# Kernel optimization log

Hardware: AMD Instinct MI355X
Metric: run time of the kernel (lower is better)

Reference implementation:

```python
import jax, jax.numpy as jnp
import numpy as np

DIM = 1024
HEADS = 8
DIM_HEAD = 64
EPS = 1e-10
LN_EPS = 1e-5


def setup_inputs() -> dict:
    key = jax.random.key(0)
    k1, k2, k3 = jax.random.split(key, 3)
    b, n = 2, 4096
    x = jax.random.normal(k1, (b, n, DIM), dtype=jnp.float32)
    ln_gamma = jnp.ones((DIM,), dtype=jnp.float32)
    ln_beta = jnp.zeros((DIM,), dtype=jnp.float32)
    w_qkv = jax.random.normal(k2, (DIM, 3 * HEADS * DIM_HEAD), dtype=jnp.float32) * (DIM ** -0.5)
    w_out = jax.random.normal(k3, (HEADS * DIM_HEAD, DIM), dtype=jnp.float32) * ((HEADS * DIM_HEAD) ** -0.5)
    return {"x": x, "ln_gamma": ln_gamma, "ln_beta": ln_beta, "w_qkv": w_qkv, "w_out": w_out}


def _layernorm(x, gamma, beta):
    mu = jnp.mean(x, axis=-1, keepdims=True)
    var = jnp.var(x, axis=-1, keepdims=True)
    return (x - mu) * jax.lax.rsqrt(var + LN_EPS) * gamma + beta


def reference(x, ln_gamma, ln_beta, w_qkv, w_out):
    b, n, _ = x.shape
    h, dh = HEADS, DIM_HEAD
    scale = dh ** -0.5

    xn = _layernorm(x, ln_gamma, ln_beta)          # prenorm
    qkv = xn @ w_qkv                               # [b, n, 3*h*dh]
    q, k, v = jnp.split(qkv, 3, axis=-1)
    # [b, n, h*dh] -> [b, h, n, dh]
    def to_heads(t):
        return t.reshape(b, n, h, dh).transpose(0, 2, 1, 3)
    q, k, v = to_heads(q), to_heads(k), to_heads(v)

    # Ring/blockwise attention with online softmax is mathematically
    # equivalent to full softmax attention with an eps in the denominator.
    sim = jnp.einsum('bhid,bhjd->bhij', q, k) * scale   # [b, h, n, n]
    causal_mask = jnp.tril(jnp.ones((n, n), dtype=bool))
    sim = jnp.where(causal_mask, sim, -jnp.finfo(sim.dtype).max)

    m = jnp.max(sim, axis=-1, keepdims=True)            # row max (stable)
    p = jnp.exp(sim - m)
    denom = jnp.sum(p, axis=-1, keepdims=True) + EPS
    attn = p / denom

    out = jnp.einsum('bhij,bhjd->bhid', attn, v)        # [b, h, n, dh]
    out = out.transpose(0, 2, 1, 3).reshape(b, n, h * dh)
    return out @ w_out                                  # [b, n, dim]
```

## Files before the change

### kernel.cpp

```cpp
#include <hip/hip_runtime.h>
#include <hip/hip_bf16.h>
#include <stdint.h>

typedef unsigned short u16;
typedef unsigned int u32;

typedef __attribute__((ext_vector_type(8))) __bf16 bf16x8;
typedef __attribute__((ext_vector_type(4))) float f32x4;
typedef __attribute__((ext_vector_type(8))) u16 u16x8;

#define DIM 1024
#define SEQ 4096
#define NTOK 8192
#define NBH 16
#define NSLOT 96

static __device__ __forceinline__ float bf2f(u16 u) {
    union { u32 u; float f; } c; c.u = ((u32)u) << 16; return c.f;
}
static __device__ __forceinline__ u16 f2bf(float f) {
    union { float f; u32 u; } c; c.f = f;
    u32 u = c.u;
    return (u16)((u + 0x7FFF + ((u >> 16) & 1)) >> 16);
}
static __device__ __forceinline__ u16 cvt_bf16(float f) {
    union { __bf16 b; u16 u; } c; c.b = (__bf16)f;
    return c.u;
}
static __device__ __forceinline__ f32x4 mfma_bf16(bf16x8 a, bf16x8 b, f32x4 c) {
    return __builtin_amdgcn_mfma_f32_16x16x32_bf16(a, b, c, 0, 0, 0);
}

typedef const __attribute__((address_space(1))) unsigned int* gptr_t;
typedef __attribute__((address_space(3))) unsigned int* lptr_t;

__global__ __launch_bounds__(256) void ln_kernel(const float* __restrict__ x,
                                                 const float* __restrict__ g,
                                                 const float* __restrict__ bta,
                                                 u16* __restrict__ xn) {
    int row = blockIdx.x;
    int tid = threadIdx.x;
    float4 v = ((const float4*)(x + (size_t)row * DIM))[tid];
    float f[4] = {v.x, v.y, v.z, v.w};
    float s = 0.f, s2 = 0.f;
#pragma unroll
    for (int i = 0; i < 4; i++) { s += f[i]; s2 += f[i] * f[i]; }
#pragma unroll
    for (int m = 1; m < 64; m <<= 1) { s += __shfl_xor(s, m); s2 += __shfl_xor(s2, m); }
    __shared__ float red[8];
    int w = tid >> 6;
    if ((tid & 63) == 0) { red[w * 2] = s; red[w * 2 + 1] = s2; }
    __syncthreads();
    s  = red[0] + red[2] + red[4] + red[6];
    s2 = red[1] + red[3] + red[5] + red[7];
    float mu = s * (1.f / DIM);
    float var = s2 * (1.f / DIM) - mu * mu;
    float rstd = rsqrtf(var + 1e-5f);
    u16 o[4];
#pragma unroll
    for (int i = 0; i < 4; i++) {
        int c = tid * 4 + i;
        o[i] = f2bf((f[i] - mu) * rstd * g[c] + bta[c]);
    }
    *(uint64_t*)(xn + (size_t)row * DIM + tid * 4) = *(uint64_t*)o;
}

__global__ __launch_bounds__(256) void transpose_kernel(const float* __restrict__ src,
                                                        u16* __restrict__ dst,
                                                        int R, int C) {
    __shared__ float t[32][33];
    int lx = threadIdx.x & 31, ly = threadIdx.x >> 5;
    int c = blockIdx.x * 32 + lx;
#pragma unroll
    for (int i = 0; i < 32; i += 8)
        t[ly + i][lx] = src[(size_t)(blockIdx.y * 32 + ly + i) * C + c];
    __syncthreads();
    int rr = blockIdx.y * 32 + lx;
#pragma unroll
    for (int i = 0; i < 32; i += 8)
        dst[(size_t)(blockIdx.x * 32 + ly + i) * R + rr] = f2bf(t[lx][ly + i]);
}

template <int K>
static __device__ __forceinline__ void gemm_core(const u16* __restrict__ A,
                                                 const u16* __restrict__ B,
                                                 int rowBase, int colBase,
                                                 u16* A_lds, u16* B_lds,
                                                 f32x4 acc[4][4]) {
    int tid = threadIdx.x;
    int lane = tid & 63;
    int l15 = lane & 15, q4 = lane >> 4;
    int w = tid >> 6;
    int wm = w >> 1, wn = w & 1;
#pragma unroll
    for (int mt = 0; mt < 4; mt++)
#pragma unroll
        for (int nt = 0; nt < 4; nt++) acc[mt][nt] = (f32x4){0.f, 0.f, 0.f, 0.f};

    char* Ab = (char*)A_lds;
    char* Bb = (char*)B_lds;

    for (int k0 = 0; k0 < K; k0 += 32) {
        __syncthreads();
#pragma unroll
        for (int i = 0; i < 2; i++) {
            int c = i * 256 + tid;
            int r = c >> 2;
            int piece = (c & 3) * 8;
            const u16* gA = A + (size_t)(rowBase + r) * K + k0 + piece;
            const u16* gB = B + (size_t)(colBase + r) * K + k0 + piece;
            unsigned ldsOff = (unsigned)(i * 4096 + w * 1024);
            __builtin_amdgcn_global_load_lds((gptr_t)gA, (lptr_t)(Ab + ldsOff), 16, 0, 0);
            __builtin_amdgcn_global_load_lds((gptr_t)gB, (lptr_t)(Bb + ldsOff), 16, 0, 0);
        }
        __syncthreads();
        bf16x8 a[4], b[4];
#pragma unroll
        for (int mt = 0; mt < 4; mt++)
            a[mt] = *(const bf16x8*)(A_lds + (wm * 64 + mt * 16 + l15) * 32 + q4 * 8);
#pragma unroll
        for (int nt = 0; nt < 4; nt++)
            b[nt] = *(const bf16x8*)(B_lds + (wn * 64 + nt * 16 + l15) * 32 + q4 * 8);
#pragma unroll
        for (int mt = 0; mt < 4; mt++)
#pragma unroll
            for (int nt = 0; nt < 4; nt++)
                acc[mt][nt] = mfma_bf16(a[mt], b[nt], acc[mt][nt]);
    }
}

__global__ __launch_bounds__(256) void gemm_qkv_kernel(const u16* __restrict__ xn,
                                                       const u16* __restrict__ wT,
                                                       u16* __restrict__ qb,
                                                       u16* __restrict__ kb,
                                                       u16* __restrict__ vbT) {
    __shared__ u16 A_lds[128 * 32];
    __shared__ u16 B_lds[128 * 32];
    f32x4 acc[4][4];
    gemm_core<1024>(xn, wT, blockIdx.x * 128, blockIdx.y * 128, A_lds, B_lds, acc);
    int lane = threadIdx.x & 63;
    int w = threadIdx.x >> 6;
    int wm = w >> 1, wn = w & 1;
    const float SC = 0.125f * 1.44269504f;
#pragma unroll
    for (int mt = 0; mt < 4; mt++) {
#pragma unroll
        for (int nt = 0; nt < 4; nt++) {
#pragma unroll
            for (int r = 0; r < 4; r++) {
                int m = blockIdx.x * 128 + wm * 64 + mt * 16 + (lane >> 4) * 4 + r;
                int n = blockIdx.y * 128 + wn * 64 + nt * 16 + (lane & 15);
                int piece = n >> 9;
                int c = n & 511;
                int h = c >> 6;
                int d = c & 63;
                int bi = m >> 12;
                int nn = m & 4095;
                int bh = bi * 8 + h;
                float av = acc[mt][nt][r];
                if (piece == 0)      qb[((size_t)(bh * SEQ + nn) << 6) + d] = f2bf(av * SC);
                else if (piece == 1) kb[((size_t)(bh * SEQ + nn) << 6) + d] = f2bf(av);
                else                 vbT[((size_t)(bh * 64 + d) << 12) + nn] = f2bf(av);
            }
        }
    }
}

__global__ __launch_bounds__(256) void gemm_out_kernel(const u16* __restrict__ aout,
                                                       const u16* __restrict__ wT,
                                                       float* __restrict__ out) {
    __shared__ u16 A_lds[128 * 32];
    __shared__ u16 B_lds[128 * 32];
    f32x4 acc[4][4];
    gemm_core<512>(aout, wT, blockIdx.x * 128, blockIdx.y * 128, A_lds, B_lds, acc);
    int lane = threadIdx.x & 63;
    int w = threadIdx.x >> 6;
    int wm = w >> 1, wn = w & 1;
#pragma unroll
    for (int mt = 0; mt < 4; mt++) {
#pragma unroll
        for (int nt = 0; nt < 4; nt++) {
#pragma unroll
            for (int r = 0; r < 4; r++) {
                int m = blockIdx.x * 128 + wm * 64 + mt * 16 + (lane >> 4) * 4 + r;
                int n = blockIdx.y * 128 + wn * 64 + nt * 16 + (lane & 15);
                out[(size_t)m * DIM + n] = acc[mt][nt][r];
            }
        }
    }
}

#define ASTR 72

__global__ __launch_bounds__(256) void attn_partial_kernel(const u16* __restrict__ qb,
                                                           const u16* __restrict__ kb,
                                                           const u16* __restrict__ vbT,
                                                           u16* __restrict__ part,
                                                           float* __restrict__ lpart) {
    __shared__ u16 K_lds[64 * ASTR];
    __shared__ u16 VT_lds[64 * ASTR];
    __shared__ u16 QP_lds[64 * ASTR];

    int idx = NBH * NSLOT - 1 - blockIdx.x;
    int bh = idx / NSLOT;
    int s  = idx - bh * NSLOT;
    int qt, ci;
    if (s < 32) { qt = s; ci = 0; }
    else        { int t = s - 32; qt = 32 + (t >> 1); ci = t & 1; }
    int kt0 = ci * 32;
    int kt1 = min(kt0 + 31, qt);

    int tid = threadIdx.x;
    int lane = tid & 63;
    int l15 = lane & 15, q4 = lane >> 4;
    int w = tid >> 6;

    const u16* Qp  = qb + ((size_t)bh * SEQ + qt * 64) * 64;
    const u16* Kp0 = kb + (size_t)bh * SEQ * 64;
    const u16* VTp = vbT + ((size_t)bh * 64) * SEQ;

#pragma unroll
    for (int i = 0; i < 2; i++) {
        int c = tid + 256 * i;
        int r = c >> 3;
        int kc = (c & 7) * 8;
        *(u16x8*)(QP_lds + r * ASTR + kc) = *(const u16x8*)(Qp + r * 64 + kc);
    }
    __syncthreads();
    bf16x8 aQ0 = *(const bf16x8*)(QP_lds + (w * 16 + l15) * ASTR + q4 * 8);
    bf16x8 aQ1 = *(const bf16x8*)(QP_lds + (w * 16 + l15) * ASTR + 32 + q4 * 8);
    __syncthreads();

    f32x4 Oacc[4];
    f32x4 l_acc = (f32x4){0.f, 0.f, 0.f, 0.f};
#pragma unroll
    for (int vt = 0; vt < 4; vt++) Oacc[vt] = (f32x4){0.f, 0.f, 0.f, 0.f};

    const __bf16 one_bf = (__bf16)1.0f;
    bf16x8 vones = {one_bf, one_bf, one_bf, one_bf, one_bf, one_bf, one_bf, one_bf};

    u16* Pw = QP_lds + w * 16 * ASTR;

    int c0 = tid, c1 = tid + 256;
    int r0 = c0 >> 3, kc0 = (c0 & 7) * 8;
    int r1 = c1 >> 3, kc1 = (c1 & 7) * 8;

    u16x8 krA0, krA1, vrA0, vrA1;
    {
        const u16* Kp = Kp0 + (size_t)kt0 * 64 * 64;
        krA0 = *(const u16x8*)(Kp + r0 * 64 + kc0);
        krA1 = *(const u16x8*)(Kp + r1 * 64 + kc1);
        vrA0 = *(const u16x8*)(VTp + (size_t)r0 * SEQ + kt0 * 64 + kc0);
        vrA1 = *(const u16x8*)(VTp + (size_t)r1 * SEQ + kt0 * 64 + kc1);
    }

    for (int kt = kt0; kt <= kt1; kt++) {
        __syncthreads();
        *(u16x8*)(K_lds + r0 * ASTR + kc0) = krA0;
        *(u16x8*)(K_lds + r1 * ASTR + kc1) = krA1;
        *(u16x8*)(VT_lds + r0 * ASTR + kc0) = vrA0;
        *(u16x8*)(VT_lds + r1 * ASTR + kc1) = vrA1;
        int ktn = (kt < kt1) ? kt + 1 : kt1;
        const u16* Kpn = Kp0 + (size_t)ktn * 64 * 64;
        u16x8 krB0 = *(const u16x8*)(Kpn + r0 * 64 + kc0);
        u16x8 krB1 = *(const u16x8*)(Kpn + r1 * 64 + kc1);
        u16x8 vrB0 = *(const u16x8*)(VTp + (size_t)r0 * SEQ + ktn * 64 + kc0);
        u16x8 vrB1 = *(const u16x8*)(VTp + (size_t)r1 * SEQ + ktn * 64 + kc1);
        __syncthreads();

        f32x4 sv[4];
#pragma unroll
        for (int nt = 0; nt < 4; nt++) {
            bf16x8 b0 = *(const bf16x8*)(K_lds + (nt * 16 + l15) * ASTR + q4 * 8);
            bf16x8 b1 = *(const bf16x8*)(K_lds + (nt * 16 + l15) * ASTR + 32 + q4 * 8);
            f32x4 z = (f32x4){0.f, 0.f, 0.f, 0.f};
            z = mfma_bf16(aQ0, b0, z);
            z = mfma_bf16(aQ1, b1, z);
            sv[nt] = z;
        }

        if (kt != qt) {
#pragma unroll
            for (int nt = 0; nt < 4; nt++)
#pragma unroll
                for (int r = 0; r < 4; r++)
                    Pw[(q4 * 4 + r) * ASTR + nt * 16 + l15] =
                        cvt_bf16(__builtin_amdgcn_exp2f(sv[nt][r]));
        } else {
#pragma unroll
            for (int nt = 0; nt < 4; nt++)
#pragma unroll
                for (int r = 0; r < 4; r++) {
                    int kg = nt * 16 + l15;
                    int qg = w * 16 + q4 * 4 + r;
                    float pv = (kg <= qg) ? __builtin_amdgcn_exp2f(sv[nt][r]) : 0.f;
                    Pw[(q4 * 4 + r) * ASTR + nt * 16 + l15] = cvt_bf16(pv);
                }
        }

        bf16x8 aP0 = *(const bf16x8*)(Pw + l15 * ASTR + q4 * 8);
        bf16x8 aP1 = *(const bf16x8*)(Pw + l15 * ASTR + 32 + q4 * 8);
        l_acc = mfma_bf16(aP0, vones, l_acc);
        l_acc = mfma_bf16(aP1, vones, l_acc);
#pragma unroll
        for (int vt = 0; vt < 4; vt++) {
            bf16x8 bV0 = *(const bf16x8*)(VT_lds + (vt * 16 + l15) * ASTR + q4 * 8);
            bf16x8 bV1 = *(const bf16x8*)(VT_lds + (vt * 16 + l15) * ASTR + 32 + q4 * 8);
            Oacc[vt] = mfma_bf16(aP0, bV0, Oacc[vt]);
            Oacc[vt] = mfma_bf16(aP1, bV1, Oacc[vt]);
        }

        krA0 = krB0; krA1 = krB1; vrA0 = vrB0; vrA1 = vrB1;
    }

    u16* po = part + (size_t)idx * 4096;
#pragma unroll
    for (int vt = 0; vt < 4; vt++)
#pragma unroll
        for (int r = 0; r < 4; r++) {
            int q = w * 16 + q4 * 4 + r;
            int d = vt * 16 + l15;
            po[q * 64 + d] = f2bf(Oacc[vt][r]);
        }
    if (l15 == 0) {
#pragma unroll
        for (int r = 0; r < 4; r++)
            lpart[(size_t)idx * 64 + w * 16 + q4 * 4 + r] = l_acc[r];
    }
}

__global__ __launch_bounds__(256) void attn_combine_kernel(const u16* __restrict__ part,
                                                           const float* __restrict__ lpart,
                                                           u16* __restrict__ aout) {
    int bid = blockIdx.x;
    int bh = bid >> 6;
    int qt = bid & 63;
    int nc = 1 + (qt >> 5);
    int sb = bh * NSLOT + (qt < 32 ? qt : 32 + (qt - 32) * 2);

    int t = threadIdx.x;
    int q = t >> 2;
    int dg = (t & 3) * 16;

    float acc[16];
#pragma unroll
    for (int j = 0; j < 16; j++) acc[j] = 0.f;
    float ll = 0.f;
    for (int ci = 0; ci < nc; ci++) {
        const u16* pp = part + (size_t)(sb + ci) * 4096 + q * 64 + dg;
        u16x8 v0 = *(const u16x8*)pp;
        u16x8 v1 = *(const u16x8*)(pp + 8);
#pragma unroll
        for (int j = 0; j < 8; j++) { acc[j] += bf2f(v0[j]); acc[8 + j] += bf2f(v1[j]); }
        ll += lpart[(size_t)(sb + ci) * 64 + q];
    }
    float inv = 1.f / (ll + 1e-10f);
    int b = bh >> 3, h = bh & 7;
    size_t row = (size_t)(b * SEQ + qt * 64 + q);
    u16 o[16];
#pragma unroll
    for (int j = 0; j < 16; j++) o[j] = f2bf(acc[j] * inv);
    u16* dst = aout + row * 512 + h * 64 + dg;
    *(u16x8*)dst = *(u16x8*)o;
    *(u16x8*)(dst + 8) = *(u16x8*)(o + 8);
}

extern "C" void kernel_launch(void* const* d_in, const int* in_sizes, int n_in,
                              void* d_out, int out_size, void* d_ws, size_t ws_size,
                              hipStream_t stream) {
    const float* x    = (const float*)d_in[0];
    const float* g    = (const float*)d_in[1];
    const float* bta  = (const float*)d_in[2];
    const float* wqkv = (const float*)d_in[3];
    const float* wout = (const float*)d_in[4];
    float* out = (float*)d_out;

    char* ws = (char*)d_ws;
    size_t off = 0;
    auto alloc = [&](size_t bytes) {
        void* p = ws + off;
        off += (bytes + 255) & ~(size_t)255;
        return p;
    };
    u16* xn    = (u16*)alloc((size_t)NTOK * DIM * 2);
    u16* wqkvT = (u16*)alloc((size_t)1536 * 1024 * 2);
    u16* woutT = (u16*)alloc((size_t)1024 * 512 * 2);
    u16* qb    = (u16*)alloc((size_t)NBH * SEQ * 64 * 2);
    u16* kb    = (u16*)alloc((size_t)NBH * SEQ * 64 * 2);
    u16* vbT   = (u16*)alloc((size_t)NBH * SEQ * 64 * 2);
    u16* part  = xn;
    float* lpart = (float*)(xn + (size_t)NBH * NSLOT * 4096);
    u16* aout  = qb;

    ln_kernel<<<NTOK, 256, 0, stream>>>(x, g, bta, xn);
    transpose_kernel<<<dim3(1536 / 32, 1024 / 32), 256, 0, stream>>>(wqkv, wqkvT, 1024, 1536);
    transpose_kernel<<<dim3(1024 / 32, 512 / 32), 256, 0, stream>>>(wout, woutT, 512, 1024);
    gemm_qkv_kernel<<<dim3(64, 12), 256, 0, stream>>>(xn, wqkvT, qb, kb, vbT);
    attn_partial_kernel<<<NBH * NSLOT, 256, 0, stream>>>(qb, kb, vbT, part, lpart);
    attn_combine_kernel<<<NBH * 64, 256, 0, stream>>>(part, lpart, aout);
    gemm_out_kernel<<<dim3(64, 8), 256, 0, stream>>>(aout, woutT, out);
}
```

Baseline: 247.1 us.

## Compute transposed S tile so P is written packed; load Q directly to registers

Swaps the MFMA operand order so the score tile comes out as K-by-Q. Each lane then holds four consecutive keys for one query row and can write P to LDS as one packed 8-byte store instead of sixteen scalar 2-byte stores. Q fragments are now loaded straight from global memory into registers, which removes a staging pass through LDS and two barriers. The change also gives P its own LDS buffer, sets an occupancy hint of 4 blocks per SM, and remaps block IDs to interleave work slots, at the risk of register pressure from the launch bound.

Result: faster. 230.6 us (-6.7%).

```diff
diff --git a/kernel.cpp b/kernel.cpp
--- a/kernel.cpp
+++ b/kernel.cpp
@@ -26,6 +26,9 @@
 static __device__ __forceinline__ u16 cvt_bf16(float f) {
     union { __bf16 b; u16 u; } c; c.b = (__bf16)f;
     return c.u;
+}
+static __device__ __forceinline__ u32 pack_bf16(float lo, float hi) {
+    return (u32)cvt_bf16(lo) | ((u32)cvt_bf16(hi) << 16);
 }
 static __device__ __forceinline__ f32x4 mfma_bf16(bf16x8 a, bf16x8 b, f32x4 c) {
     return __builtin_amdgcn_mfma_f32_16x16x32_bf16(a, b, c, 0, 0, 0);
@@ -191,17 +194,20 @@
 }
 
 #define ASTR 72
-
-__global__ __launch_bounds__(256) void attn_partial_kernel(const u16* __restrict__ qb,
-                                                           const u16* __restrict__ kb,
-                                                           const u16* __restrict__ vbT,
-                                                           u16* __restrict__ part,
-                                                           float* __restrict__ lpart) {
+#define PSTR 72
+
+__global__ __launch_bounds__(256, 4) void attn_partial_kernel(const u16* __restrict__ qb,
+                                                              const u16* __restrict__ kb,
+                                                              const u16* __restrict__ vbT,
+                                                              u16* __restrict__ part,
+                                                              float* __restrict__ lpart) {
     __shared__ u16 K_lds[64 * ASTR];
     __shared__ u16 VT_lds[64 * ASTR];
-    __shared__ u16 QP_lds[64 * ASTR];
-
-    int idx = NBH * NSLOT - 1 - blockIdx.x;
+    __shared__ u16 P_lds[4 * 16 * PSTR];
+
+    int bid = blockIdx.x;
+    int bs = (bid & 7) * 192 + (bid >> 3);
+    int idx = NBH * NSLOT - 1 - bs;
     int bh = idx / NSLOT;
     int s  = idx - bh * NSLOT;
     int qt, ci;
@@ -212,24 +218,15 @@
 
     int tid = threadIdx.x;
     int lane = tid & 63;
-    int l15 = lane & 15, q4 = lane >> 4;
+    int l15 = lane & 15, g = lane >> 4;
     int w = tid >> 6;
 
-    const u16* Qp  = qb + ((size_t)bh * SEQ + qt * 64) * 64;
     const u16* Kp0 = kb + (size_t)bh * SEQ * 64;
     const u16* VTp = vbT + ((size_t)bh * 64) * SEQ;
 
-#pragma unroll
-    for (int i = 0; i < 2; i++) {
-        int c = tid + 256 * i;
-        int r = c >> 3;
-        int kc = (c & 7) * 8;
-        *(u16x8*)(QP_lds + r * ASTR + kc) = *(const u16x8*)(Qp + r * 64 + kc);
-    }
-    __syncthreads();
-    bf16x8 aQ0 = *(const bf16x8*)(QP_lds + (w * 16 + l15) * ASTR + q4 * 8);
-    bf16x8 aQ1 = *(const bf16x8*)(QP_lds + (w * 16 + l15) * ASTR + 32 + q4 * 8);
-    __syncthreads();
+    const u16* Qp = qb + ((size_t)bh * SEQ + qt * 64 + w * 16 + l15) * 64;
+    bf16x8 bQ0 = *(const bf16x8*)(Qp + g * 8);
+    bf16x8 bQ1 = *(const bf16x8*)(Qp + 32 + g * 8);
 
     f32x4 Oacc[4];
     f32x4 l_acc = (f32x4){0.f, 0.f, 0.f, 0.f};
@@ -239,7 +236,7 @@
     const __bf16 one_bf = (__bf16)1.0f;
     bf16x8 vones = {one_bf, one_bf, one_bf, one_bf, one_bf, one_bf, one_bf, one_bf};
 
-    u16* Pw = QP_lds + w * 16 * ASTR;
+    u16* Pw = P_lds + w * 16 * PSTR;
 
     int c0 = tid, c1 = tid + 256;
     int r0 = c0 >> 3, kc0 = (c0 & 7) * 8;
@@ -270,42 +267,52 @@
 
         f32x4 sv[4];
 #pragma unroll
-        for (int nt = 0; nt < 4; nt++) {
-            bf16x8 b0 = *(const bf16x8*)(K_lds + (nt * 16 + l15) * ASTR + q4 * 8);
-            bf16x8 b1 = *(const bf16x8*)(K_lds + (nt * 16 + l15) * ASTR + 32 + q4 * 8);
+        for (int mt = 0; mt < 4; mt++) {
+            bf16x8 a0 = *(const bf16x8*)(K_lds + (mt * 16 + l15) * ASTR + g * 8);
+            bf16x8 a1 = *(const bf16x8*)(K_lds + (mt * 16 + l15) * ASTR + 32 + g * 8);
             f32x4 z = (f32x4){0.f, 0.f, 0.f, 0.f};
-            z = mfma_bf16(aQ0, b0, z);
-            z = mfma_bf16(aQ1, b1, z);
-            sv[nt] = z;
+            z = mfma_bf16(a0, bQ0, z);
+            z = mfma_bf16(a1, bQ1, z);
+            sv[mt] = z;
         }
 
         if (kt != qt) {
 #pragma unroll
-            for (int nt = 0; nt < 4; nt++)
-#pragma unroll
-                for (int r = 0; r < 4; r++)
-                    Pw[(q4 * 4 + r) * ASTR + nt * 16 + l15] =
-                        cvt_bf16(__builtin_amdgcn_exp2f(sv[nt][r]));
+            for (int mt = 0; mt < 4; mt++) {
+                float p0 = __builtin_amdgcn_exp2f(sv[mt][0]);
+                float p1 = __builtin_amdgcn_exp2f(sv[mt][1]);
+                float p2 = __builtin_amdgcn_exp2f(sv[mt][2]);
+                float p3 = __builtin_amdgcn_exp2f(sv[mt][3]);
+                uint2 t;
+                t.x = pack_bf16(p0, p1);
+                t.y = pack_bf16(p2, p3);
+                *(uint2*)(Pw + l15 * PSTR + mt * 16 + g * 4) = t;
+            }
         } else {
-#pragma unroll
-            for (int nt = 0; nt < 4; nt++)
+            int qg = w * 16 + l15;
+#pragma unroll
+            for (int mt = 0; mt < 4; mt++) {
+                float p[4];
 #pragma unroll
                 for (int r = 0; r < 4; r++) {
-                    int kg = nt * 16 + l15;
-                    int qg = w * 16 + q4 * 4 + r;
-                    float pv = (kg <= qg) ? __builtin_amdgcn_exp2f(sv[nt][r]) : 0.f;
-                    Pw[(q4 * 4 + r) * ASTR + nt * 16 + l15] = cvt_bf16(pv);
+                    int kg = mt * 16 + g * 4 + r;
+                    p[r] = (kg <= qg) ? __builtin_amdgcn_exp2f(sv[mt][r]) : 0.f;
                 }
-        }
-
-        bf16x8 aP0 = *(const bf16x8*)(Pw + l15 * ASTR + q4 * 8);
-        bf16x8 aP1 = *(const bf16x8*)(Pw + l15 * ASTR + 32 + q4 * 8);
+                uint2 t;
+                t.x = pack_bf16(p[0], p[1]);
+                t.y = pack_bf16(p[2], p[3]);
+                *(uint2*)(Pw + l15 * PSTR + mt * 16 + g * 4) = t;
+            }
+        }
+
+        bf16x8 aP0 = *(const bf16x8*)(Pw + l15 * PSTR + g * 8);
+        bf16x8 aP1 = *(const bf16x8*)(Pw + l15 * PSTR + 32 + g * 8);
         l_acc = mfma_bf16(aP0, vones, l_acc);
         l_acc = mfma_bf16(aP1, vones, l_acc);
 #pragma unroll
         for (int vt = 0; vt < 4; vt++) {
-            bf16x8 bV0 = *(const bf16x8*)(VT_lds + (vt * 16 + l15) * ASTR + q4 * 8);
-            bf16x8 bV1 = *(const bf16x8*)(VT_lds + (vt * 16 + l15) * ASTR + 32 + q4 * 8);
+            bf16x8 bV0 = *(const bf16x8*)(VT_lds + (vt * 16 + l15) * ASTR + g * 8);
+            bf16x8 bV1 = *(const bf16x8*)(VT_lds + (vt * 16 + l15) * ASTR + 32 + g * 8);
             Oacc[vt] = mfma_bf16(aP0, bV0, Oacc[vt]);
             Oacc[vt] = mfma_bf16(aP1, bV1, Oacc[vt]);
         }
@@ -318,14 +325,14 @@
     for (int vt = 0; vt < 4; vt++)
 #pragma unroll
         for (int r = 0; r < 4; r++) {
-            int q = w * 16 + q4 * 4 + r;
+            int q = w * 16 + g * 4 + r;
             int d = vt * 16 + l15;
             po[q * 64 + d] = f2bf(Oacc[vt][r]);
         }
     if (l15 == 0) {
 #pragma unroll
         for (int r = 0; r < 4; r++)
-            lpart[(size_t)idx * 64 + w * 16 + q4 * 4 + r] = l_acc[r];
+            lpart[(size_t)idx * 64 + w * 16 + g * 4 + r] = l_acc[r];
     }
 }
 
```
